# Kernel optimization log

Measured on AMD Instinct MI355X. Metric: run time of the kernel, lower is better.

Reference implementation:

```python
import jax, jax.numpy as jnp
import numpy as np

N = 4096
D_IN = 1024
D_OUT = 512
DENSITY = 0.005
LRELU_ALPHA = 0.2  # tf.nn.leaky_relu default


def _make_adj(key):
    # sparse binary adjacency, symmetric, with self-loops (dense 0/1 float mask)
    a = (jax.random.uniform(key, (N, N)) < DENSITY).astype(jnp.float32)
    a = jnp.maximum(a, a.T)
    a = jnp.maximum(a, jnp.eye(N, dtype=jnp.float32))
    return a


def setup_inputs() -> dict:
    key = jax.random.key(0)
    ks = jax.random.split(key, 7)
    x = jax.random.normal(ks[0], (N, D_IN), dtype=jnp.float32)
    adj = _make_adj(ks[1])
    # glorot-ish scales
    Wf = jax.random.normal(ks[2], (D_IN, D_OUT), dtype=jnp.float32) * (1.0 / np.sqrt(D_IN))
    a1 = jax.random.normal(ks[3], (D_OUT, 1), dtype=jnp.float32) * (1.0 / np.sqrt(D_OUT))
    b1 = jnp.zeros((1,), dtype=jnp.float32)
    a2 = jax.random.normal(ks[4], (D_OUT, 1), dtype=jnp.float32) * (1.0 / np.sqrt(D_OUT))
    b2 = jnp.zeros((1,), dtype=jnp.float32)
    W = jax.random.normal(ks[5], (D_IN, D_OUT), dtype=jnp.float32) * (1.0 / np.sqrt(D_IN))
    return {"x": x, "adj": adj, "Wf": Wf, "a1": a1, "b1": b1, "a2": a2, "b2": b2, "W": W}


def reference(x, adj, Wf, a1, b1, a2, b2, W):
    # dropout = 0 (inference) -> identity; coef dropout skipped for determinism
    mask = adj != 0.0
    # conv1d(kernel=1) == pointwise linear
    seq_fts = x @ Wf                      # [N, D_OUT]
    f1 = seq_fts @ a1 + b1                # [N, 1]
    f2 = seq_fts @ a2 + b2                # [N, 1]
    # sparse logits: adj_ij * f1_i + adj_ij * f2_j on edges
    logits = adj * f1 + adj * f2.T        # [N, N]
    lrelu = jnp.where(logits >= 0, logits, LRELU_ALPHA * logits)
    # sparse softmax over edge entries per row
    masked = jnp.where(mask, lrelu, -jnp.inf)
    coefs = jax.nn.softmax(masked, axis=1)
    coefs = jnp.where(mask, coefs, 0.0)
    # symmetrize: (coefs + coefs^T)/2
    coefs = (coefs + coefs.T) * 0.5
    # coefs_I = diag(rowsum^0) = I  (pow(x,0)==1)
    coefs_mat = coefs + jnp.eye(N, dtype=coefs.dtype)
    rowsum = jnp.sum(coefs_mat, axis=1, keepdims=True)   # [N,1], >= 1
    d_inv_sqrt = rowsum ** -0.5
    d_inv_inverse = d_inv_sqrt ** -1.0
    inf_int = jnp.isinf(d_inv_sqrt).astype(jnp.float32)
    d = (d_inv_inverse + inf_int) ** -1.0 - inf_int
    d = jnp.sum(d, axis=1)                # [N]
    d_mat = jnp.diag(d)                   # [N,N] diagonal matrix
    # NOTE: original uses ELEMENTWISE multiply with the diag matrix (faithful):
    support_mat = (coefs_mat * d_mat).T * d_mat   # effectively diagonal
    pre_sup = x @ W                       # [N, D_OUT]
    out = support_mat @ pre_sup           # [N, D_OUT]
    return jax.nn.relu(out)
```

## Files before the change

### kernel.cpp

```cpp
#include <hip/hip_runtime.h>
#include <stdint.h>
#include <math.h>

#define NN 4096
#define DIN 1024
#define DOUT 512
#define ALPHA 0.2f

typedef __attribute__((ext_vector_type(8))) short short8;
typedef __attribute__((ext_vector_type(4))) float f32x4;

__device__ __forceinline__ unsigned short f2bf(float f) {
    uint32_t u = __float_as_uint(f);
    u += 0x7fffu + ((u >> 16) & 1u);
    return (unsigned short)(u >> 16);
}

__device__ __forceinline__ void async16(const void* g, void* l) {
    __builtin_amdgcn_global_load_lds(
        (const __attribute__((address_space(1))) uint32_t*)g,
        (__attribute__((address_space(3))) uint32_t*)l, 16, 0, 0);
}

__global__ __launch_bounds__(256) void k_prep(const float* __restrict__ W,
                                              const float* __restrict__ Wf,
                                              const float* __restrict__ a1,
                                              const float* __restrict__ a2,
                                              unsigned short* __restrict__ wt,
                                              float* __restrict__ wa1,
                                              float* __restrict__ wa2) {
    int tid = threadIdx.x;
    if (blockIdx.x < 256) {
        int bx = blockIdx.x & 7, gy = blockIdx.x >> 3;
        int n = bx * 64 + (tid & 63);
        int g = gy * 4 + (tid >> 6);
        float v[8];
#pragma unroll
        for (int j = 0; j < 8; ++j) v[j] = W[(size_t)(g * 8 + j) * DOUT + n];
        union { unsigned short u[8]; uint4 q; } pk;
#pragma unroll
        for (int j = 0; j < 8; ++j) pk.u[j] = f2bf(v[j]);
        int sw = (n >> 1) & 3;
        int p  = (g & ~3) | ((g & 3) ^ sw);
        *(uint4*)(wt + (size_t)n * DIN + p * 8) = pk.q;
    } else {
        int row  = (blockIdx.x - 256) * 4 + (tid >> 6);
        int lane = tid & 63;
        const float* wr = Wf + (size_t)row * DOUT;
        float s1 = 0.f, s2 = 0.f;
        for (int k = lane; k < DOUT; k += 64) {
            float w = wr[k];
            s1 += w * a1[k];
            s2 += w * a2[k];
        }
        for (int off = 32; off; off >>= 1) {
            s1 += __shfl_down(s1, off);
            s2 += __shfl_down(s2, off);
        }
        if (lane == 0) { wa1[row] = s1; wa2[row] = s2; }
    }
}

__global__ __launch_bounds__(256) void k_fx(const float* __restrict__ x,
    const float* __restrict__ wa1, const float* __restrict__ wa2,
    const float* __restrict__ b1, const float* __restrict__ b2,
    float* __restrict__ f1, float* __restrict__ f2,
    unsigned short* __restrict__ xb) {
    int row  = blockIdx.x * 4 + (threadIdx.x >> 6);
    int lane = threadIdx.x & 63;
    const float* xr = x + (size_t)row * DIN + lane * 16;
    float xv[16];
    *(float4*)&xv[0]  = *(const float4*)(xr);
    *(float4*)&xv[4]  = *(const float4*)(xr + 4);
    *(float4*)&xv[8]  = *(const float4*)(xr + 8);
    *(float4*)&xv[12] = *(const float4*)(xr + 12);
    asm volatile("" ::: "memory");
    const float* w1 = wa1 + lane * 16;
    const float* w2 = wa2 + lane * 16;
    float s1 = 0.f, s2 = 0.f;
#pragma unroll
    for (int j = 0; j < 16; ++j) {
        s1 += xv[j] * w1[j];
        s2 += xv[j] * w2[j];
    }
    union { unsigned short u[8]; uint4 q; } pk0, pk1;
#pragma unroll
    for (int j = 0; j < 8; ++j) { pk0.u[j] = f2bf(xv[j]); pk1.u[j] = f2bf(xv[8 + j]); }
    int sw = (row >> 1) & 3;
    int g0 = lane * 2, g1 = lane * 2 + 1;
    int p0 = (g0 & ~3) | ((g0 & 3) ^ sw);
    int p1 = (g1 & ~3) | ((g1 & 3) ^ sw);
    unsigned short* xrow = xb + (size_t)row * DIN;
    *(uint4*)(xrow + p0 * 8) = pk0.q;
    *(uint4*)(xrow + p1 * 8) = pk1.q;
    for (int off = 32; off; off >>= 1) {
        s1 += __shfl_down(s1, off);
        s2 += __shfl_down(s2, off);
    }
    if (lane == 0) { f1[row] = s1 + b1[0]; f2[row] = s2 + b2[0]; }
}

__global__ __launch_bounds__(256) void k_stats(const float* __restrict__ adj,
                                               const float* __restrict__ f1,
                                               const float* __restrict__ f2,
                                               float* __restrict__ rZ_out,
                                               unsigned short* __restrict__ bits16) {
    int tid = threadIdx.x;
    int row0 = blockIdx.x * 2;
    const float4* a0 = (const float4*)(adj + (size_t)row0 * NN);
    const float4* a1 = (const float4*)(adj + (size_t)(row0 + 1) * NN);
    float4 v0 = a0[tid];       float4 v1 = a0[tid + 256];
    float4 v2 = a0[tid + 512]; float4 v3 = a0[tid + 768];
    float4 v4 = a1[tid];       float4 v5 = a1[tid + 256];
    float4 v6 = a1[tid + 512]; float4 v7 = a1[tid + 768];
    asm volatile("" ::: "memory");
    unsigned int m0 = 0, m1 = 0;
#define MB(M, V, J)                                            \
    M |= (((V).x != 0.f) ? 1u : 0u) << (4 * (J));              \
    M |= (((V).y != 0.f) ? 1u : 0u) << (4 * (J) + 1);          \
    M |= (((V).z != 0.f) ? 1u : 0u) << (4 * (J) + 2);          \
    M |= (((V).w != 0.f) ? 1u : 0u) << (4 * (J) + 3);
    MB(m0, v0, 0) MB(m0, v1, 1) MB(m0, v2, 2) MB(m0, v3, 3)
    MB(m1, v4, 0) MB(m1, v5, 1) MB(m1, v6, 2) MB(m1, v7, 3)
#undef MB
    bits16[(size_t)row0 * 256 + tid]       = (unsigned short)m0;
    bits16[(size_t)row0 * 256 + 256 + tid] = (unsigned short)m1;
    float f10 = f1[row0], f11 = f1[row0 + 1];
    float z0 = 0.f, z1 = 0.f;
    unsigned int w = m0;
    while (w) {
        int b = __builtin_ctz(w); w &= w - 1;
        float l = f10 + f2[4 * tid + 1024 * (b >> 2) + (b & 3)];
        z0 += __expf((l >= 0.f) ? l : ALPHA * l);
    }
    w = m1;
    while (w) {
        int b = __builtin_ctz(w); w &= w - 1;
        float l = f11 + f2[4 * tid + 1024 * (b >> 2) + (b & 3)];
        z1 += __expf((l >= 0.f) ? l : ALPHA * l);
    }
    int lane = tid & 63, wid = tid >> 6;
    for (int off = 32; off; off >>= 1) {
        z0 += __shfl_down(z0, off);
        z1 += __shfl_down(z1, off);
    }
    __shared__ float red[8];
    if (lane == 0) { red[wid] = z0; red[4 + wid] = z1; }
    __syncthreads();
    if (tid == 0) rZ_out[row0]     = 1.0f / (red[0] + red[1] + red[2] + red[3]);
    if (tid == 1) rZ_out[row0 + 1] = 1.0f / (red[4] + red[5] + red[6] + red[7]);
}

__global__ __launch_bounds__(256) void k_s(const unsigned long long* __restrict__ bits,
                                           const float* __restrict__ f1,
                                           const float* __restrict__ f2,
                                           const float* __restrict__ rZ,
                                           float* __restrict__ s_out) {
    int row  = blockIdx.x * 4 + (threadIdx.x >> 6);
    int lane = threadIdx.x & 63;
    unsigned long long w = bits[(size_t)row * 64 + lane];
    float f2r = f2[row];
    float sum = 0.f;
    while (w) {
        int b = __builtin_ctzll(w);
        w &= w - 1;
        int j = 16 * lane + 4 * (b >> 4) + 1024 * ((b >> 2) & 3) + (b & 3);
        float l = f1[j] + f2r;
        float e = (l >= 0.f) ? l : ALPHA * l;
        sum += __expf(e) * rZ[j];
    }
    for (int off = 32; off; off >>= 1) sum += __shfl_down(sum, off);
    if (lane == 0) {
        float l   = f1[row] + f2r;
        float e   = (l >= 0.f) ? l : ALPHA * l;
        float cjj = __expf(e) * rZ[row];
        s_out[row] = (cjj + 1.0f) / (1.5f + 0.5f * sum);
    }
}

__global__ __launch_bounds__(256) void k_gemm(const unsigned short* __restrict__ xb,
                                              const unsigned short* __restrict__ wt,
                                              const float* __restrict__ s,
                                              float* __restrict__ out) {
    __shared__ __align__(16) unsigned short As[2][128][32];
    __shared__ __align__(16) unsigned short Bs[2][64][32];
    int lid = blockIdx.y * gridDim.x + blockIdx.x;
    int xcd = lid & 7, idx = lid >> 3;
    int by = xcd * 4 + (idx & 3);
    int bx = idx >> 2;
    int bm = by * 128, bn = bx * 64;

    int tid = threadIdx.x, wid = tid >> 6, lane = tid & 63;
    int wr = wid >> 1, wc = wid & 1;

    int srow = lane >> 2, sg = lane & 3;
    const unsigned short* ga0 = xb + (size_t)(bm + wid * 32 + srow) * DIN + sg * 8;
    const unsigned short* gb0 = wt + (size_t)(bn + wid * 16 + srow) * DIN + sg * 8;

    int r15 = lane & 15, gl = lane >> 4;
    int gofs = (gl ^ ((r15 >> 1) & 3)) * 8;

    f32x4 acc[4][2] = {};

#define STAGE(BUF, K0) do {                                              \
        async16(ga0 + (K0),            &As[BUF][wid * 32][0]);           \
        async16(ga0 + (K0) + 16 * DIN, &As[BUF][wid * 32 + 16][0]);      \
        async16(gb0 + (K0),            &Bs[BUF][wid * 16][0]);           \
    } while (0)

#define COMPUTE(BUF) do {                                                \
        const unsigned short* pa = &As[BUF][wr * 64 + r15][gofs];        \
        const unsigned short* pb = &Bs[BUF][wc * 32 + r15][gofs];        \
        short8 af0 = *(const short8*)(pa);                               \
        short8 af1 = *(const short8*)(pa + 16 * 32);                     \
        short8 af2 = *(const short8*)(pa + 32 * 32);                     \
        short8 af3 = *(const short8*)(pa + 48 * 32);                     \
        short8 bf0 = *(const short8*)(pb);                               \
        short8 bf1 = *(const short8*)(pb + 16 * 32);                     \
        acc[0][0] = __builtin_amdgcn_mfma_f32_16x16x32_bf16(af0, bf0, acc[0][0], 0, 0, 0); \
        acc[0][1] = __builtin_amdgcn_mfma_f32_16x16x32_bf16(af0, bf1, acc[0][1], 0, 0, 0); \
        acc[1][0] = __builtin_amdgcn_mfma_f32_16x16x32_bf16(af1, bf0, acc[1][0], 0, 0, 0); \
        acc[1][1] = __builtin_amdgcn_mfma_f32_16x16x32_bf16(af1, bf1, acc[1][1], 0, 0, 0); \
        acc[2][0] = __builtin_amdgcn_mfma_f32_16x16x32_bf16(af2, bf0, acc[2][0], 0, 0, 0); \
        acc[2][1] = __builtin_amdgcn_mfma_f32_16x16x32_bf16(af2, bf1, acc[2][1], 0, 0, 0); \
        acc[3][0] = __builtin_amdgcn_mfma_f32_16x16x32_bf16(af3, bf0, acc[3][0], 0, 0, 0); \
        acc[3][1] = __builtin_amdgcn_mfma_f32_16x16x32_bf16(af3, bf1, acc[3][1], 0, 0, 0); \
    } while (0)

    STAGE(0, 0);
    asm volatile("s_waitcnt vmcnt(0)" ::: "memory");
    __syncthreads();
    int cur = 0;
    for (int t = 0; t < (DIN / 32) - 1; ++t) {
        STAGE(cur ^ 1, (t + 1) * 32);
        COMPUTE(cur);
        asm volatile("s_waitcnt vmcnt(0)" ::: "memory");
        __syncthreads();
        cur ^= 1;
    }
    COMPUTE(cur);

#pragma unroll
    for (int mi = 0; mi < 4; ++mi) {
        int crow0 = bm + wr * 64 + mi * 16 + gl * 4;
#pragma unroll
        for (int ni = 0; ni < 2; ++ni) {
            int ccol = bn + wc * 32 + ni * 16 + r15;
#pragma unroll
            for (int r = 0; r < 4; ++r) {
                int row = crow0 + r;
                float v = acc[mi][ni][r] * s[row];
                out[(size_t)row * DOUT + ccol] = fmaxf(v, 0.f);
            }
        }
    }
#undef STAGE
#undef COMPUTE
}

extern "C" void kernel_launch(void* const* d_in, const int* in_sizes, int n_in,
                              void* d_out, int out_size, void* d_ws, size_t ws_size,
                              hipStream_t stream) {
    const float* x   = (const float*)d_in[0];
    const float* adj = (const float*)d_in[1];
    const float* Wf  = (const float*)d_in[2];
    const float* a1  = (const float*)d_in[3];
    const float* b1  = (const float*)d_in[4];
    const float* a2  = (const float*)d_in[5];
    const float* b2  = (const float*)d_in[6];
    const float* W   = (const float*)d_in[7];
    float* out = (float*)d_out;

    char* w = (char*)d_ws;
    float* wa1 = (float*)(w + 0);
    float* wa2 = (float*)(w + 4096);
    float* f1  = (float*)(w + 16384);
    float* f2  = (float*)(w + 32768);
    float* rZ  = (float*)(w + 49152);
    float* s   = (float*)(w + 65536);
    unsigned short* bits16 = (unsigned short*)(w + 98304);
    unsigned short* xb = (unsigned short*)(w + 2195456);
    unsigned short* wt = (unsigned short*)(w + 10584064);

    k_prep<<<512, 256, 0, stream>>>(W, Wf, a1, a2, wt, wa1, wa2);
    k_fx<<<1024, 256, 0, stream>>>(x, wa1, wa2, b1, b2, f1, f2, xb);
    k_stats<<<2048, 256, 0, stream>>>(adj, f1, f2, rZ, bits16);
    k_s<<<1024, 256, 0, stream>>>((const unsigned long long*)bits16, f1, f2, rZ, s);
    dim3 gg(8, 32);
    k_gemm<<<gg, 256, 0, stream>>>(xb, wt, s, out);
}
```

Baseline: 51.81 us.

## Merge adjacency bitmask build with x projection; split softmax denominator pass

The adjacency-to-bitmask pass no longer depends on f1/f2, so it now runs in the same launch as the x projection and bf16 conversion, using disjoint block ranges. This lets the 64MB adjacency read overlap with the x read. The row softmax denominator moves to a new lightweight kernel that reads the compact bitmask, mirroring k_s. The kernel count stays the same, but the bitmask is now re-read from global memory once more.

```diff
diff --git a/kernel.cpp b/kernel.cpp
--- a/kernel.cpp
+++ b/kernel.cpp
@@ -61,94 +61,88 @@
     }
 }
 
-__global__ __launch_bounds__(256) void k_fx(const float* __restrict__ x,
+__global__ __launch_bounds__(256) void k_maskfx(const float* __restrict__ adj,
+    const float* __restrict__ x,
     const float* __restrict__ wa1, const float* __restrict__ wa2,
     const float* __restrict__ b1, const float* __restrict__ b2,
     float* __restrict__ f1, float* __restrict__ f2,
-    unsigned short* __restrict__ xb) {
+    unsigned short* __restrict__ xb,
+    unsigned short* __restrict__ bits16) {
+    int tid = threadIdx.x;
+    if (blockIdx.x < 2048) {
+        int row0 = blockIdx.x * 2;
+        const float4* a0 = (const float4*)(adj + (size_t)row0 * NN);
+        const float4* a1v = (const float4*)(adj + (size_t)(row0 + 1) * NN);
+        float4 v0 = a0[tid];        float4 v1 = a0[tid + 256];
+        float4 v2 = a0[tid + 512];  float4 v3 = a0[tid + 768];
+        float4 v4 = a1v[tid];       float4 v5 = a1v[tid + 256];
+        float4 v6 = a1v[tid + 512]; float4 v7 = a1v[tid + 768];
+        asm volatile("" ::: "memory");
+        unsigned int m0 = 0, m1 = 0;
+#define MB(M, V, J)                                            \
+        M |= (((V).x != 0.f) ? 1u : 0u) << (4 * (J));          \
+        M |= (((V).y != 0.f) ? 1u : 0u) << (4 * (J) + 1);      \
+        M |= (((V).z != 0.f) ? 1u : 0u) << (4 * (J) + 2);      \
+        M |= (((V).w != 0.f) ? 1u : 0u) << (4 * (J) + 3);
+        MB(m0, v0, 0) MB(m0, v1, 1) MB(m0, v2, 2) MB(m0, v3, 3)
+        MB(m1, v4, 0) MB(m1, v5, 1) MB(m1, v6, 2) MB(m1, v7, 3)
+#undef MB
+        bits16[(size_t)row0 * 256 + tid]       = (unsigned short)m0;
+        bits16[(size_t)row0 * 256 + 256 + tid] = (unsigned short)m1;
+    } else {
+        int row  = (blockIdx.x - 2048) * 4 + (tid >> 6);
+        int lane = tid & 63;
+        const float* xr = x + (size_t)row * DIN + lane * 16;
+        float xv[16];
+        *(float4*)&xv[0]  = *(const float4*)(xr);
+        *(float4*)&xv[4]  = *(const float4*)(xr + 4);
+        *(float4*)&xv[8]  = *(const float4*)(xr + 8);
+        *(float4*)&xv[12] = *(const float4*)(xr + 12);
+        asm volatile("" ::: "memory");
+        const float* w1 = wa1 + lane * 16;
+        const float* w2 = wa2 + lane * 16;
+        float s1 = 0.f, s2 = 0.f;
+#pragma unroll
+        for (int j = 0; j < 16; ++j) {
+            s1 += xv[j] * w1[j];
+            s2 += xv[j] * w2[j];
+        }
+        union { unsigned short u[8]; uint4 q; } pk0, pk1;
+#pragma unroll
+        for (int j = 0; j < 8; ++j) { pk0.u[j] = f2bf(xv[j]); pk1.u[j] = f2bf(xv[8 + j]); }
+        int sw = (row >> 1) & 3;
+        int g0 = lane * 2, g1 = lane * 2 + 1;
+        int p0 = (g0 & ~3) | ((g0 & 3) ^ sw);
+        int p1 = (g1 & ~3) | ((g1 & 3) ^ sw);
+        unsigned short* xrow = xb + (size_t)row * DIN;
+        *(uint4*)(xrow + p0 * 8) = pk0.q;
+        *(uint4*)(xrow + p1 * 8) = pk1.q;
+        for (int off = 32; off; off >>= 1) {
+            s1 += __shfl_down(s1, off);
+            s2 += __shfl_down(s2, off);
+        }
+        if (lane == 0) { f1[row] = s1 + b1[0]; f2[row] = s2 + b2[0]; }
+    }
+}
+
+__global__ __launch_bounds__(256) void k_z(const unsigned long long* __restrict__ bits,
+                                           const float* __restrict__ f1,
+                                           const float* __restrict__ f2,
+                                           float* __restrict__ rZ_out) {
     int row  = blockIdx.x * 4 + (threadIdx.x >> 6);
     int lane = threadIdx.x & 63;
-    const float* xr = x + (size_t)row * DIN + lane * 16;
-    float xv[16];
-    *(float4*)&xv[0]  = *(const float4*)(xr);
-    *(float4*)&xv[4]  = *(const float4*)(xr + 4);
-    *(float4*)&xv[8]  = *(const float4*)(xr + 8);
-    *(float4*)&xv[12] = *(const float4*)(xr + 12);
-    asm volatile("" ::: "memory");
-    const float* w1 = wa1 + lane * 16;
-    const float* w2 = wa2 + lane * 16;
-    float s1 = 0.f, s2 = 0.f;
-#pragma unroll
-    for (int j = 0; j < 16; ++j) {
-        s1 += xv[j] * w1[j];
-        s2 += xv[j] * w2[j];
-    }
-    union { unsigned short u[8]; uint4 q; } pk0, pk1;
-#pragma unroll
-    for (int j = 0; j < 8; ++j) { pk0.u[j] = f2bf(xv[j]); pk1.u[j] = f2bf(xv[8 + j]); }
-    int sw = (row >> 1) & 3;
-    int g0 = lane * 2, g1 = lane * 2 + 1;
-    int p0 = (g0 & ~3) | ((g0 & 3) ^ sw);
-    int p1 = (g1 & ~3) | ((g1 & 3) ^ sw);
-    unsigned short* xrow = xb + (size_t)row * DIN;
-    *(uint4*)(xrow + p0 * 8) = pk0.q;
-    *(uint4*)(xrow + p1 * 8) = pk1.q;
-    for (int off = 32; off; off >>= 1) {
-        s1 += __shfl_down(s1, off);
-        s2 += __shfl_down(s2, off);
-    }
-    if (lane == 0) { f1[row] = s1 + b1[0]; f2[row] = s2 + b2[0]; }
-}
-
-__global__ __launch_bounds__(256) void k_stats(const float* __restrict__ adj,
-                                               const float* __restrict__ f1,
-                                               const float* __restrict__ f2,
-                                               float* __restrict__ rZ_out,
-                                               unsigned short* __restrict__ bits16) {
-    int tid = threadIdx.x;
-    int row0 = blockIdx.x * 2;
-    const float4* a0 = (const float4*)(adj + (size_t)row0 * NN);
-    const float4* a1 = (const float4*)(adj + (size_t)(row0 + 1) * NN);
-    float4 v0 = a0[tid];       float4 v1 = a0[tid + 256];
-    float4 v2 = a0[tid + 512]; float4 v3 = a0[tid + 768];
-    float4 v4 = a1[tid];       float4 v5 = a1[tid + 256];
-    float4 v6 = a1[tid + 512]; float4 v7 = a1[tid + 768];
-    asm volatile("" ::: "memory");
-    unsigned int m0 = 0, m1 = 0;
-#define MB(M, V, J)                                            \
-    M |= (((V).x != 0.f) ? 1u : 0u) << (4 * (J));              \
-    M |= (((V).y != 0.f) ? 1u : 0u) << (4 * (J) + 1);          \
-    M |= (((V).z != 0.f) ? 1u : 0u) << (4 * (J) + 2);          \
-    M |= (((V).w != 0.f) ? 1u : 0u) << (4 * (J) + 3);
-    MB(m0, v0, 0) MB(m0, v1, 1) MB(m0, v2, 2) MB(m0, v3, 3)
-    MB(m1, v4, 0) MB(m1, v5, 1) MB(m1, v6, 2) MB(m1, v7, 3)
-#undef MB
-    bits16[(size_t)row0 * 256 + tid]       = (unsigned short)m0;
-    bits16[(size_t)row0 * 256 + 256 + tid] = (unsigned short)m1;
-    float f10 = f1[row0], f11 = f1[row0 + 1];
-    float z0 = 0.f, z1 = 0.f;
-    unsigned int w = m0;
+    unsigned long long w = bits[(size_t)row * 64 + lane];
+    float f1r = f1[row];
+    float z = 0.f;
     while (w) {
-        int b = __builtin_ctz(w); w &= w - 1;
-        float l = f10 + f2[4 * tid + 1024 * (b >> 2) + (b & 3)];
-        z0 += __expf((l >= 0.f) ? l : ALPHA * l);
-    }
-    w = m1;
-    while (w) {
-        int b = __builtin_ctz(w); w &= w - 1;
-        float l = f11 + f2[4 * tid + 1024 * (b >> 2) + (b & 3)];
-        z1 += __expf((l >= 0.f) ? l : ALPHA * l);
-    }
-    int lane = tid & 63, wid = tid >> 6;
-    for (int off = 32; off; off >>= 1) {
-        z0 += __shfl_down(z0, off);
-        z1 += __shfl_down(z1, off);
-    }
-    __shared__ float red[8];
-    if (lane == 0) { red[wid] = z0; red[4 + wid] = z1; }
-    __syncthreads();
-    if (tid == 0) rZ_out[row0]     = 1.0f / (red[0] + red[1] + red[2] + red[3]);
-    if (tid == 1) rZ_out[row0 + 1] = 1.0f / (red[4] + red[5] + red[6] + red[7]);
+        int b = __builtin_ctzll(w);
+        w &= w - 1;
+        int j = 16 * lane + 4 * (b >> 4) + 1024 * ((b >> 2) & 3) + (b & 3);
+        float l = f1r + f2[j];
+        z += __expf((l >= 0.f) ? l : ALPHA * l);
+    }
+    for (int off = 32; off; off >>= 1) z += __shfl_down(z, off);
+    if (lane == 0) rZ_out[row] = 1.0f / z;
 }
 
 __global__ __launch_bounds__(256) void k_s(const unsigned long long* __restrict__ bits,
@@ -283,8 +277,8 @@
     unsigned short* wt = (unsigned short*)(w + 10584064);
 
     k_prep<<<512, 256, 0, stream>>>(W, Wf, a1, a2, wt, wa1, wa2);
-    k_fx<<<1024, 256, 0, stream>>>(x, wa1, wa2, b1, b2, f1, f2, xb);
-    k_stats<<<2048, 256, 0, stream>>>(adj, f1, f2, rZ, bits16);
+    k_maskfx<<<3072, 256, 0, stream>>>(adj, x, wa1, wa2, b1, b2, f1, f2, xb, bits16);
+    k_z<<<1024, 256, 0, stream>>>((const unsigned long long*)bits16, f1, f2, rZ);
     k_s<<<1024, 256, 0, stream>>>((const unsigned long long*)bits16, f1, f2, rZ, s);
     dim3 gg(8, 32);
     k_gemm<<<gg, 256, 0, stream>>>(xb, wt, s, out);
```

After: 51.06 us. Within noise of the previous version (-1.4%).
